# Optimization experiments

Hardware: AMD Instinct MI355X
Metric: run time of the kernel (lower is better)

## Reference

```python
import jax, jax.numpy as jnp
import numpy as np

B, D, S, F, C, H, OUT = 4, 60, 512, 158, 64, 128, 1
LN_EPS = 1e-5


def setup_inputs() -> dict:
    key = jax.random.key(0)
    ks = jax.random.split(key, 12)
    g = lambda k, shape, s=0.05: jax.random.normal(k, shape, dtype=jnp.float32) * s
    return dict(
        x=jax.random.normal(ks[0], (B, D, S, F), dtype=jnp.float32),
        feature_mask=jax.random.randint(ks[1], (B, D, S), 0, 2).astype(bool),
        wq=g(ks[2], (F, C)), bq=jnp.zeros((C,), jnp.float32),
        wk=g(ks[3], (F, C)), bk=jnp.zeros((C,), jnp.float32),
        wv=g(ks[4], (F, C)), bv=jnp.zeros((C,), jnp.float32),
        ln_g=jnp.ones((F + C,), jnp.float32), ln_b=jnp.zeros((F + C,), jnp.float32),
        w_ih=g(ks[5], (3 * H, F + C)), w_hh=g(ks[6], (3 * H, H)),
        b_ih=jnp.zeros((3 * H,), jnp.float32), b_hh=jnp.zeros((3 * H,), jnp.float32),
        w1=g(ks[7], (H, H // 2)), b1=jnp.zeros((H // 2,), jnp.float32),
        w2=g(ks[8], (H // 2, OUT)), b2=jnp.zeros((OUT,), jnp.float32),
    )


def reference(x, feature_mask, wq, bq, wk, bk, wv, bv, ln_g, ln_b,
              w_ih, w_hh, b_ih, b_hh, w1, b1, w2, b2):
    b, d, s, f = x.shape
    c = wq.shape[1]
    h_dim = w_hh.shape[1]

    # --- market context attention, vectorized over (batch, days) ---
    Q = x @ wq + bq            # (B,D,S,C)
    K = x @ wk + bk
    V = x @ wv + bv
    scores = jnp.einsum('bdsc,bdtc->bdst', Q, K) / jnp.sqrt(jnp.float32(c))
    scores = jnp.where(feature_mask[:, :, None, :], scores, -1e9)  # mask keys
    attn = jax.nn.softmax(scores, axis=-1)
    ctx = jnp.einsum('bdst,bdtc->bdsc', attn, V)       # (B,D,S,C)
    ctx = jnp.where(feature_mask[..., None], ctx, 0.0)  # mask queries
    denom = jnp.maximum(feature_mask.sum(axis=2), 1).astype(x.dtype)  # (B,D)
    market = ctx.sum(axis=2) / denom[..., None]         # (B,D,C)

    # --- concat + layernorm ---
    aug = jnp.concatenate(
        [x, jnp.broadcast_to(market[:, :, None, :], (b, d, s, c))], axis=-1)
    mu = aug.mean(-1, keepdims=True)
    var = aug.var(-1, keepdims=True)
    aug = (aug - mu) / jnp.sqrt(var + LN_EPS) * ln_g + ln_b  # (B,D,S,F+C)

    # --- GRU over days, batch = B*S independent sequences ---
    seq = aug.transpose(1, 0, 2, 3).reshape(d, b * s, f + c)  # (D, N, F+C)
    x_proj = seq @ w_ih.T + b_ih                               # (D, N, 3H)

    def step(h, xp):
        hp = h @ w_hh.T + b_hh
        xr, xz, xn = jnp.split(xp, 3, axis=-1)
        hr, hz, hn = jnp.split(hp, 3, axis=-1)
        r = jax.nn.sigmoid(xr + hr)
        z = jax.nn.sigmoid(xz + hz)
        n = jnp.tanh(xn + r * hn)
        return (1.0 - z) * n + z * h, None

    h0 = jnp.zeros((b * s, h_dim), x.dtype)
    h_last, _ = jax.lax.scan(step, h0, x_proj)  # last-step output
    h_last = h_last.reshape(b, s, h_dim)

    # --- output head (dropout inactive in eval) ---
    hid = jax.nn.relu(h_last @ w1 + b1)
    return hid @ w2 + b2  # (B, S, OUT)
```

## Files before the change

kernel.cpp:

```cpp
#include <hip/hip_runtime.h>
#include <hip/hip_bf16.h>
#include <math.h>

#define BB 4
#define DD 60
#define SS 512
#define FF 158
#define CC 64
#define HH 128
#define FC 222
#define G3 384
#define NN 2048
#define BDN 240

typedef _Float16 f16x8 __attribute__((ext_vector_type(8)));
typedef float f32x4 __attribute__((ext_vector_type(4)));

__device__ __forceinline__ float sigmoidf_(float x){ return 1.0f/(1.0f+__expf(-x)); }
__device__ __forceinline__ float tanhf_(float x){
    float e = __expf(-2.0f*fabsf(x));
    float t = (1.0f - e)/(1.0f + e);
    return copysignf(t, x);
}

__global__ void prep_kernel(const float* __restrict__ w_ih,
                            const float* __restrict__ wq, const float* __restrict__ wk,
                            const float* __restrict__ wv,
                            _Float16* __restrict__ wf16, _Float16* __restrict__ wqkv){
    int idx = blockIdx.x*256 + threadIdx.x;
    if (idx < 384*224){
        int n = idx / 224, k = idx % 224;
        wf16[idx] = (k < FC) ? (_Float16)w_ih[n*FC + k] : (_Float16)0.0f;
    } else {
        int i2 = idx - 384*224;
        if (i2 < 192*160){
            int n = i2 / 160, k = i2 % 160;
            float v = 0.0f;
            if (k < FF){
                if (n < 64)       v = wq[k*CC + n];
                else if (n < 128) v = wk[k*CC + (n-64)];
                else              v = wv[k*CC + (n-128)];
            }
            wqkv[i2] = (_Float16)v;
        }
    }
}

__global__ __launch_bounds__(256) void qkv_kernel(const float* __restrict__ x,
                           const _Float16* __restrict__ wqkv,
                           const float* __restrict__ bq, const float* __restrict__ bk,
                           const float* __restrict__ bv,
                           _Float16* __restrict__ Qh, _Float16* __restrict__ Kh,
                           float* __restrict__ V){
    __shared__ _Float16 xa[5][64][40];
    int tid  = threadIdx.x;
    int lane = tid & 63, wv = tid >> 6;
    int col  = lane & 15, quad = lane >> 4;
    int row0 = blockIdx.x * 64;

    f16x8 bfr[3][5];
    #pragma unroll
    for (int nt = 0; nt < 3; ++nt){
        int n = wv*48 + nt*16 + col;
        #pragma unroll
        for (int kq = 0; kq < 5; ++kq)
            bfr[nt][kq] = *(const f16x8*)&wqkv[n*160 + kq*32 + quad*8];
    }

    for (int i = tid; i < 64*160; i += 256){
        int r = i / 160, k = i % 160;
        float v = (k < FF) ? x[(size_t)(row0 + r)*FF + k] : 0.0f;
        xa[k >> 5][r][k & 31] = (_Float16)v;
    }
    __syncthreads();

    float bias[3];
    #pragma unroll
    for (int nt = 0; nt < 3; ++nt){
        int n = wv*48 + nt*16 + col;
        bias[nt] = (n < 64) ? bq[n] : (n < 128 ? bk[n-64] : bv[n-128]);
    }

    #pragma unroll 1
    for (int mt = 0; mt < 4; ++mt){
        f16x8 a[5];
        #pragma unroll
        for (int kq = 0; kq < 5; ++kq)
            a[kq] = *(const f16x8*)&xa[kq][mt*16 + col][quad*8];
        #pragma unroll
        for (int nt = 0; nt < 3; ++nt){
            f32x4 c = {0.0f, 0.0f, 0.0f, 0.0f};
            #pragma unroll
            for (int kq = 0; kq < 5; ++kq)
                c = __builtin_amdgcn_mfma_f32_16x16x32_f16(a[kq], bfr[nt][kq], c, 0, 0, 0);
            int n = wv*48 + nt*16 + col;
            #pragma unroll
            for (int reg = 0; reg < 4; ++reg){
                int row = row0 + mt*16 + quad*4 + reg;
                float val = c[reg] + bias[nt];
                if (n < 64)       Qh[(size_t)row*CC + n]       = (_Float16)val;
                else if (n < 128) Kh[(size_t)row*CC + (n-64)]  = (_Float16)val;
                else              V [(size_t)row*CC + (n-128)] = val;
            }
        }
    }
}

__global__ __launch_bounds__(512) void attn_kernel(const _Float16* __restrict__ Qh,
                                                   const _Float16* __restrict__ Kh,
                                                   const int* __restrict__ mask,
                                                   float* __restrict__ Wg){
    __shared__ _Float16 kf[2][512][32];
    __shared__ float w_sh[512];
    __shared__ float mk_lds[512];

    int tid  = threadIdx.x;
    int bd   = blockIdx.x;
    int lane = tid & 63, wv = tid >> 6;
    int col  = lane & 15, quad = lane >> 4;

    const _Float16* qb = Qh + (size_t)(bd*SS)*CC;
    const _Float16* kb = Kh + (size_t)(bd*SS)*CC;

    {
        int t = tid;
        w_sh[t] = 0.0f;
        mk_lds[t] = (mask[bd*SS + t] != 0) ? 1.0f : 0.0f;
    }
    for (int i = tid; i < 4096; i += 512){
        int t = i >> 3, ch = i & 7;
        *(f16x8*)&kf[ch >> 2][t][(ch & 3)*8] = *(const f16x8*)&kb[t*CC + ch*8];
    }

    f16x8 a0[4], a1[4];
    #pragma unroll
    for (int af = 0; af < 4; ++af){
        int row = wv*64 + af*16 + col;
        a0[af] = *(const f16x8*)&qb[row*CC + quad*8];
        a1[af] = *(const f16x8*)&qb[row*CC + 32 + quad*8];
    }
    __syncthreads();

    float lacc[4][4] = {{0,0,0,0},{0,0,0,0},{0,0,0,0},{0,0,0,0}};
    #pragma unroll 2
    for (int kt = 0; kt < 32; ++kt){
        f16x8 b0 = *(const f16x8*)&kf[0][kt*16 + col][quad*8];
        f16x8 b1 = *(const f16x8*)&kf[1][kt*16 + col][quad*8];
        float mkv = mk_lds[kt*16 + col];
        #pragma unroll
        for (int af = 0; af < 4; ++af){
            f32x4 c = {0.0f, 0.0f, 0.0f, 0.0f};
            c = __builtin_amdgcn_mfma_f32_16x16x32_f16(a0[af], b0, c, 0, 0, 0);
            c = __builtin_amdgcn_mfma_f32_16x16x32_f16(a1[af], b1, c, 0, 0, 0);
            #pragma unroll
            for (int reg = 0; reg < 4; ++reg)
                lacc[af][reg] += __expf(c[reg]*0.125f) * mkv;
        }
    }
    float crv[4][4];
    #pragma unroll
    for (int af = 0; af < 4; ++af){
        #pragma unroll
        for (int reg = 0; reg < 4; ++reg){
            float l = lacc[af][reg];
            l += __shfl_xor(l, 1, 64);
            l += __shfl_xor(l, 2, 64);
            l += __shfl_xor(l, 4, 64);
            l += __shfl_xor(l, 8, 64);
            int row = wv*64 + af*16 + quad*4 + reg;
            crv[af][reg] = mk_lds[row] / l;
        }
    }

    #pragma unroll 2
    for (int kt = 0; kt < 32; ++kt){
        f16x8 b0 = *(const f16x8*)&kf[0][kt*16 + col][quad*8];
        f16x8 b1 = *(const f16x8*)&kf[1][kt*16 + col][quad*8];
        float s = 0.0f;
        #pragma unroll
        for (int af = 0; af < 4; ++af){
            f32x4 c = {0.0f, 0.0f, 0.0f, 0.0f};
            c = __builtin_amdgcn_mfma_f32_16x16x32_f16(a0[af], b0, c, 0, 0, 0);
            c = __builtin_amdgcn_mfma_f32_16x16x32_f16(a1[af], b1, c, 0, 0, 0);
            #pragma unroll
            for (int reg = 0; reg < 4; ++reg)
                s = fmaf(__expf(c[reg]*0.125f), crv[af][reg], s);
        }
        s += __shfl_xor(s, 16, 64);
        s += __shfl_xor(s, 32, 64);
        if (quad == 0)
            atomicAdd(&w_sh[kt*16 + col], s);
    }
    __syncthreads();
    Wg[bd*SS + tid] = w_sh[tid];
}

__global__ void market_kernel(const float* __restrict__ Wg, const float* __restrict__ V,
                              const int* __restrict__ mask, float* __restrict__ market){
    int bd = blockIdx.x;
    int c  = threadIdx.x;
    int cnt = 0;
    #pragma unroll
    for (int j = 0; j < 8; ++j) cnt += (mask[bd*SS + c + j*64] != 0) ? 1 : 0;
    #pragma unroll
    for (int o = 1; o < 64; o <<= 1) cnt += __shfl_xor(cnt, o, 64);
    float acc = 0.0f;
    for (int t = 0; t < SS; ++t){
        float mkt = (mask[bd*SS + t] != 0) ? 1.0f : 0.0f;
        acc = fmaf(Wg[bd*SS + t]*mkt, V[(size_t)(bd*SS + t)*CC + c], acc);
    }
    int dn = cnt < 1 ? 1 : cnt;
    market[bd*CC + c] = acc / (float)dn;
}

__global__ __launch_bounds__(512, 2) void xproj_kernel(const float* __restrict__ x,
                             const float* __restrict__ market,
                             const float* __restrict__ ln_g, const float* __restrict__ ln_b,
                             const _Float16* __restrict__ wf16, const float* __restrict__ b_ih,
                             _Float16* __restrict__ XP){
    __shared__ _Float16 aug[7][64][32];
    int tid  = threadIdx.x;
    int lane = tid & 63, wv = tid >> 6;
    int col  = lane & 15, quad = lane >> 4;
    int row0 = blockIdx.x * 64;

    f16x8 bfr[3][7];
    #pragma unroll
    for (int nt = 0; nt < 3; ++nt){
        int n = wv*48 + nt*16 + col;
        #pragma unroll
        for (int kq = 0; kq < 7; ++kq)
            bfr[nt][kq] = *(const f16x8*)&wf16[n*224 + kq*32 + quad*8];
    }

    {
        int wrow = wv*8 + (lane >> 3);
        int g    = lane & 7;
        int row  = row0 + wrow;
        int d = row / NN, n = row % NN;
        int b = n >> 9, s = n & 511;
        const float* xr = &x[((size_t)((b*DD + d)*SS) + s)*FF];
        const float* mr = &market[(b*DD + d)*CC];
        float v[28];
        float sum = 0.0f, sq = 0.0f;
        #pragma unroll
        for (int j = 0; j < 28; ++j){
            int f = g + 8*j;
            float vv = 0.0f;
            if (f < FF) vv = xr[f];
            else if (f < FC) vv = mr[f - FF];
            v[j] = vv;
            sum += vv; sq += vv*vv;
        }
        sum += __shfl_xor(sum,1,64); sq += __shfl_xor(sq,1,64);
        sum += __shfl_xor(sum,2,64); sq += __shfl_xor(sq,2,64);
        sum += __shfl_xor(sum,4,64); sq += __shfl_xor(sq,4,64);
        float mu   = sum * (1.0f/222.0f);
        float var  = sq * (1.0f/222.0f) - mu*mu;
        float rstd = rsqrtf(var + 1e-5f);
        #pragma unroll
        for (int j = 0; j < 28; ++j){
            int f = g + 8*j;
            float val = (f < FC) ? ((v[j]-mu)*rstd*ln_g[f] + ln_b[f]) : 0.0f;
            aug[f>>5][wrow][f&31] = (_Float16)val;
        }
    }
    __syncthreads();

    float bias[3];
    #pragma unroll
    for (int nt = 0; nt < 3; ++nt) bias[nt] = b_ih[wv*48 + nt*16 + col];
    #pragma unroll 1
    for (int mt = 0; mt < 4; ++mt){
        f16x8 a[7];
        #pragma unroll
        for (int kq = 0; kq < 7; ++kq)
            a[kq] = *(const f16x8*)&aug[kq][mt*16 + col][quad*8];
        #pragma unroll
        for (int nt = 0; nt < 3; ++nt){
            f32x4 c = {0.0f, 0.0f, 0.0f, 0.0f};
            #pragma unroll
            for (int kq = 0; kq < 7; ++kq)
                c = __builtin_amdgcn_mfma_f32_16x16x32_f16(a[kq], bfr[nt][kq], c, 0, 0, 0);
            int nn = wv*48 + nt*16 + col;
            #pragma unroll
            for (int reg = 0; reg < 4; ++reg){
                int m = quad*4 + reg;
                XP[(size_t)(row0 + mt*16 + m)*G3 + nn] = (_Float16)(c[reg] + bias[nt]);
            }
        }
    }
}

__global__ __launch_bounds__(256, 2) void gru_kernel(const _Float16* __restrict__ XP,
                                                     const float* __restrict__ w_hh,
                                                     const float* __restrict__ b_hh,
                                                     const float* __restrict__ w1, const float* __restrict__ b1,
                                                     const float* __restrict__ w2, const float* __restrict__ b2,
                                                     float* __restrict__ out){
    __shared__ _Float16 h_hf[16][136];
    __shared__ float hp_lds[4][392];
    __shared__ float h_f32[4][132];

    int tid  = threadIdx.x;
    int lane = tid & 63, wv = tid >> 6;
    int col  = lane & 15, quad = lane >> 4;
    int row0 = blockIdx.x * 4;

    for (int i = tid; i < 16*136; i += 256) ((_Float16*)h_hf)[i] = (_Float16)0.0f;
    for (int i = tid; i < 4*132; i += 256) ((float*)h_f32)[i] = 0.0f;

    f16x8 bfr[6][4];
    #pragma unroll
    for (int nt = 0; nt < 6; ++nt){
        int n = wv*96 + nt*16 + col;
        #pragma unroll
        for (int kq = 0; kq < 4; ++kq){
            const float* wr = w_hh + n*HH + kq*32 + quad*8;
            f16x8 v;
            #pragma unroll
            for (int j = 0; j < 8; ++j) v[j] = (_Float16)wr[j];
            bfr[nt][kq] = v;
        }
    }

    int cc = tid & 127, sgrp = tid >> 7;
    float bhr = b_hh[cc], bhz = b_hh[128 + cc], bhn = b_hh[256 + cc];

    float xc[2][3], xn_[2][3];
    {
        const _Float16* base = XP + (size_t)(row0)*G3 + cc;
        #pragma unroll
        for (int sp = 0; sp < 2; ++sp){
            int seq = sgrp + 2*sp;
            xc[sp][0] = (float)base[seq*G3];
            xc[sp][1] = (float)base[seq*G3 + 128];
            xc[sp][2] = (float)base[seq*G3 + 256];
        }
    }
    __syncthreads();

    for (int d = 0; d < DD; ++d){
        if (d < DD-1){
            const _Float16* base = XP + ((size_t)(d+1)*NN + row0)*G3 + cc;
            #pragma unroll
            for (int sp = 0; sp < 2; ++sp){
                int seq = sgrp + 2*sp;
                xn_[sp][0] = (float)base[seq*G3];
                xn_[sp][1] = (float)base[seq*G3 + 128];
                xn_[sp][2] = (float)base[seq*G3 + 256];
            }
        }
        f16x8 a[4];
        #pragma unroll
        for (int kq = 0; kq < 4; ++kq)
            a[kq] = *(const f16x8*)&h_hf[col][kq*32 + quad*8];
        f32x4 acc[6];
        #pragma unroll
        for (int nt = 0; nt < 6; ++nt){
            f32x4 c = {0.0f, 0.0f, 0.0f, 0.0f};
            #pragma unroll
            for (int kq = 0; kq < 4; ++kq)
                c = __builtin_amdgcn_mfma_f32_16x16x32_f16(a[kq], bfr[nt][kq], c, 0, 0, 0);
            acc[nt] = c;
        }
        if (quad == 0){
            #pragma unroll
            for (int nt = 0; nt < 6; ++nt){
                int n0 = wv*96 + nt*16 + col;
                #pragma unroll
                for (int reg = 0; reg < 4; ++reg)
                    hp_lds[reg][n0] = acc[nt][reg];
            }
        }
        __syncthreads();
        #pragma unroll
        for (int sp = 0; sp < 2; ++sp){
            int seq = sgrp + 2*sp;
            float hr = hp_lds[seq][cc]       + bhr;
            float hz = hp_lds[seq][cc + 128] + bhz;
            float hn = hp_lds[seq][cc + 256] + bhn;
            float r  = sigmoidf_(xc[sp][0] + hr);
            float z  = sigmoidf_(xc[sp][1] + hz);
            float n  = tanhf_(xc[sp][2] + r*hn);
            float ho = h_f32[seq][cc];
            float hnew = (1.0f - z)*n + z*ho;
            h_f32[seq][cc] = hnew;
            h_hf[seq][cc]  = (_Float16)hnew;
        }
        #pragma unroll
        for (int sp = 0; sp < 2; ++sp){
            xc[sp][0] = xn_[sp][0]; xc[sp][1] = xn_[sp][1]; xc[sp][2] = xn_[sp][2];
        }
        __syncthreads();
    }

    if (tid < 64){
        int c2 = tid;
        #pragma unroll 1
        for (int r = 0; r < 4; ++r){
            float a0 = 0.0f, a1 = 0.0f;
            #pragma unroll 8
            for (int k = 0; k < 64; ++k){
                a0 = fmaf(h_f32[r][k],      w1[k*64 + c2],        a0);
                a1 = fmaf(h_f32[r][64 + k], w1[(64 + k)*64 + c2], a1);
            }
            float hid = fmaxf(a0 + a1 + b1[c2], 0.0f);
            float o = hid * w2[c2];
            #pragma unroll
            for (int off = 1; off < 64; off <<= 1) o += __shfl_xor(o, off, 64);
            if (c2 == 0) out[row0 + r] = o + b2[0];
        }
    }
}

extern "C" void kernel_launch(void* const* d_in, const int* in_sizes, int n_in,
                              void* d_out, int out_size, void* d_ws, size_t ws_size,
                              hipStream_t stream) {
    const float* x    = (const float*)d_in[0];
    const int*   mask = (const int*)d_in[1];
    const float* wq   = (const float*)d_in[2];
    const float* bq   = (const float*)d_in[3];
    const float* wk   = (const float*)d_in[4];
    const float* bk   = (const float*)d_in[5];
    const float* wv   = (const float*)d_in[6];
    const float* bv   = (const float*)d_in[7];
    const float* ln_g = (const float*)d_in[8];
    const float* ln_b = (const float*)d_in[9];
    const float* w_ih = (const float*)d_in[10];
    const float* w_hh = (const float*)d_in[11];
    const float* b_ih = (const float*)d_in[12];
    const float* b_hh = (const float*)d_in[13];
    const float* w1   = (const float*)d_in[14];
    const float* b1   = (const float*)d_in[15];
    const float* w2   = (const float*)d_in[16];
    const float* b2   = (const float*)d_in[17];

    float* ws = (float*)d_ws;
    _Float16* Qh  = (_Float16*)ws;
    _Float16* Kh  = (_Float16*)(ws + 3932160);
    float*    V   = ws + 7864320;
    float*    Wg  = ws + 15728640;
    _Float16* XP  = (_Float16*)ws;
    float* market = ws + 23592960;
    _Float16* wf16= (_Float16*)(ws + 23608320);
    _Float16* wqkv= (_Float16*)(ws + 23651328);

    prep_kernel<<<456, 256, 0, stream>>>(w_ih, wq, wk, wv, wf16, wqkv);
    qkv_kernel<<<1920, 256, 0, stream>>>(x, wqkv, bq, bk, bv, Qh, Kh, V);
    attn_kernel<<<240, 512, 0, stream>>>(Qh, Kh, mask, Wg);
    market_kernel<<<240, 64, 0, stream>>>(Wg, V, mask, market);
    xproj_kernel<<<1920, 512, 0, stream>>>(x, market, ln_g, ln_b, wf16, b_ih, XP);
    gru_kernel<<<512, 256, 0, stream>>>(XP, w_hh, b_hh, w1, b1, w2, b2, (float*)d_out);
}
```

Before: 399.7 us.

## Fuse market reduction into attention and restructure GRU step to one barrier

Folds the separate market-averaging kernel into the tail of the attention kernel, which removes the Wg round-trip through global memory and one launch. The GRU recurrence now gives each wave the r/z/n gate columns for its own 32 hidden units. Per-step hidden state is double-buffered in LDS and kept in registers, cutting one __syncthreads per step. The recurrent weights are pre-converted to fp16 in the prep kernel, so the GRU loads them with vector loads instead of converting from float.

```diff
diff --git a/kernel.cpp b/kernel.cpp
--- a/kernel.cpp
+++ b/kernel.cpp
@@ -25,24 +25,27 @@
 
 __global__ void prep_kernel(const float* __restrict__ w_ih,
                             const float* __restrict__ wq, const float* __restrict__ wk,
-                            const float* __restrict__ wv,
-                            _Float16* __restrict__ wf16, _Float16* __restrict__ wqkv){
+                            const float* __restrict__ wv, const float* __restrict__ w_hh,
+                            _Float16* __restrict__ wf16, _Float16* __restrict__ wqkv,
+                            _Float16* __restrict__ whh16){
     int idx = blockIdx.x*256 + threadIdx.x;
     if (idx < 384*224){
         int n = idx / 224, k = idx % 224;
         wf16[idx] = (k < FC) ? (_Float16)w_ih[n*FC + k] : (_Float16)0.0f;
+    } else if (idx < 384*224 + 192*160){
+        int i2 = idx - 384*224;
+        int n = i2 / 160, k = i2 % 160;
+        float v = 0.0f;
+        if (k < FF){
+            if (n < 64)       v = wq[k*CC + n];
+            else if (n < 128) v = wk[k*CC + (n-64)];
+            else              v = wv[k*CC + (n-128)];
+        }
+        wqkv[i2] = (_Float16)v;
     } else {
-        int i2 = idx - 384*224;
-        if (i2 < 192*160){
-            int n = i2 / 160, k = i2 % 160;
-            float v = 0.0f;
-            if (k < FF){
-                if (n < 64)       v = wq[k*CC + n];
-                else if (n < 128) v = wk[k*CC + (n-64)];
-                else              v = wv[k*CC + (n-128)];
-            }
-            wqkv[i2] = (_Float16)v;
-        }
+        int i3 = idx - (384*224 + 192*160);
+        if (i3 < 384*128)
+            whh16[i3] = (_Float16)w_hh[i3];
     }
 }
 
@@ -109,7 +112,8 @@
 __global__ __launch_bounds__(512) void attn_kernel(const _Float16* __restrict__ Qh,
                                                    const _Float16* __restrict__ Kh,
                                                    const int* __restrict__ mask,
-                                                   float* __restrict__ Wg){
+                                                   const float* __restrict__ V,
+                                                   float* __restrict__ market){
     __shared__ _Float16 kf[2][512][32];
     __shared__ float w_sh[512];
     __shared__ float mk_lds[512];
@@ -192,25 +196,30 @@
             atomicAdd(&w_sh[kt*16 + col], s);
     }
     __syncthreads();
-    Wg[bd*SS + tid] = w_sh[tid];
-}
-
-__global__ void market_kernel(const float* __restrict__ Wg, const float* __restrict__ V,
-                              const int* __restrict__ mask, float* __restrict__ market){
-    int bd = blockIdx.x;
-    int c  = threadIdx.x;
-    int cnt = 0;
-    #pragma unroll
-    for (int j = 0; j < 8; ++j) cnt += (mask[bd*SS + c + j*64] != 0) ? 1 : 0;
-    #pragma unroll
-    for (int o = 1; o < 64; o <<= 1) cnt += __shfl_xor(cnt, o, 64);
-    float acc = 0.0f;
-    for (int t = 0; t < SS; ++t){
-        float mkt = (mask[bd*SS + t] != 0) ? 1.0f : 0.0f;
-        acc = fmaf(Wg[bd*SS + t]*mkt, V[(size_t)(bd*SS + t)*CC + c], acc);
-    }
-    int dn = cnt < 1 ? 1 : cnt;
-    market[bd*CC + c] = acc / (float)dn;
+
+    float* msum = (float*)kf;
+    {
+        int c = tid & 63, grp = tid >> 6;
+        const float* vb = V + (size_t)(bd*SS)*CC;
+        float acc = 0.0f;
+        int t0 = grp*64;
+        #pragma unroll 4
+        for (int t = t0; t < t0 + 64; ++t)
+            acc = fmaf(w_sh[t]*mk_lds[t], vb[(size_t)t*CC + c], acc);
+        msum[grp*64 + c] = acc;
+    }
+    __syncthreads();
+    if (tid < 64){
+        float s = 0.0f;
+        #pragma unroll
+        for (int g = 0; g < 8; ++g) s += msum[g*64 + tid];
+        float cnt = 0.0f;
+        #pragma unroll
+        for (int j = 0; j < 8; ++j) cnt += mk_lds[tid + 64*j];
+        #pragma unroll
+        for (int o = 1; o < 64; o <<= 1) cnt += __shfl_xor(cnt, o, 64);
+        market[bd*CC + tid] = s / fmaxf(cnt, 1.0f);
+    }
 }
 
 __global__ __launch_bounds__(512, 2) void xproj_kernel(const float* __restrict__ x,
@@ -293,13 +302,13 @@
 }
 
 __global__ __launch_bounds__(256, 2) void gru_kernel(const _Float16* __restrict__ XP,
-                                                     const float* __restrict__ w_hh,
+                                                     const _Float16* __restrict__ whh16,
                                                      const float* __restrict__ b_hh,
                                                      const float* __restrict__ w1, const float* __restrict__ b1,
                                                      const float* __restrict__ w2, const float* __restrict__ b2,
                                                      float* __restrict__ out){
-    __shared__ _Float16 h_hf[16][136];
-    __shared__ float hp_lds[4][392];
+    __shared__ _Float16 hfrag[2][4][16][32];
+    __shared__ float hp_sh[4][3][4][32];
     __shared__ float h_f32[4][132];
 
     int tid  = threadIdx.x;
@@ -307,93 +316,94 @@
     int col  = lane & 15, quad = lane >> 4;
     int row0 = blockIdx.x * 4;
 
-    for (int i = tid; i < 16*136; i += 256) ((_Float16*)h_hf)[i] = (_Float16)0.0f;
-    for (int i = tid; i < 4*132; i += 256) ((float*)h_f32)[i] = 0.0f;
-
-    f16x8 bfr[6][4];
-    #pragma unroll
-    for (int nt = 0; nt < 6; ++nt){
-        int n = wv*96 + nt*16 + col;
-        #pragma unroll
-        for (int kq = 0; kq < 4; ++kq){
-            const float* wr = w_hh + n*HH + kq*32 + quad*8;
-            f16x8 v;
-            #pragma unroll
-            for (int j = 0; j < 8; ++j) v[j] = (_Float16)wr[j];
-            bfr[nt][kq] = v;
-        }
-    }
-
-    int cc = tid & 127, sgrp = tid >> 7;
-    float bhr = b_hh[cc], bhz = b_hh[128 + cc], bhn = b_hh[256 + cc];
-
+    for (int i = tid; i < 2*4*16*32; i += 256) ((_Float16*)hfrag)[i] = (_Float16)0.0f;
+
+    f16x8 bfr[3][2][4];
+    #pragma unroll
+    for (int g = 0; g < 3; ++g){
+        #pragma unroll
+        for (int hf = 0; hf < 2; ++hf){
+            int n = g*128 + wv*32 + hf*16 + col;
+            #pragma unroll
+            for (int kq = 0; kq < 4; ++kq)
+                bfr[g][hf][kq] = *(const f16x8*)&whh16[(size_t)n*HH + kq*32 + quad*8];
+        }
+    }
+
+    int u  = lane & 31;
+    int cc = wv*32 + u;
+    int sb = lane >> 5;
+    float bh0 = b_hh[cc], bh1 = b_hh[128 + cc], bh2 = b_hh[256 + cc];
+
+    float hcur[2] = {0.0f, 0.0f};
     float xc[2][3], xn_[2][3];
-    {
-        const _Float16* base = XP + (size_t)(row0)*G3 + cc;
-        #pragma unroll
-        for (int sp = 0; sp < 2; ++sp){
-            int seq = sgrp + 2*sp;
-            xc[sp][0] = (float)base[seq*G3];
-            xc[sp][1] = (float)base[seq*G3 + 128];
-            xc[sp][2] = (float)base[seq*G3 + 256];
-        }
+    #pragma unroll
+    for (int j = 0; j < 2; ++j){
+        int seq = j*2 + sb;
+        const _Float16* base = XP + (size_t)(row0 + seq)*G3 + cc;
+        xc[j][0] = (float)base[0];
+        xc[j][1] = (float)base[128];
+        xc[j][2] = (float)base[256];
     }
     __syncthreads();
 
     for (int d = 0; d < DD; ++d){
         if (d < DD-1){
-            const _Float16* base = XP + ((size_t)(d+1)*NN + row0)*G3 + cc;
-            #pragma unroll
-            for (int sp = 0; sp < 2; ++sp){
-                int seq = sgrp + 2*sp;
-                xn_[sp][0] = (float)base[seq*G3];
-                xn_[sp][1] = (float)base[seq*G3 + 128];
-                xn_[sp][2] = (float)base[seq*G3 + 256];
+            #pragma unroll
+            for (int j = 0; j < 2; ++j){
+                int seq = j*2 + sb;
+                const _Float16* base = XP + ((size_t)(d+1)*NN + row0 + seq)*G3 + cc;
+                xn_[j][0] = (float)base[0];
+                xn_[j][1] = (float)base[128];
+                xn_[j][2] = (float)base[256];
             }
         }
+        int rb = d & 1;
         f16x8 a[4];
         #pragma unroll
         for (int kq = 0; kq < 4; ++kq)
-            a[kq] = *(const f16x8*)&h_hf[col][kq*32 + quad*8];
-        f32x4 acc[6];
-        #pragma unroll
-        for (int nt = 0; nt < 6; ++nt){
-            f32x4 c = {0.0f, 0.0f, 0.0f, 0.0f};
-            #pragma unroll
-            for (int kq = 0; kq < 4; ++kq)
-                c = __builtin_amdgcn_mfma_f32_16x16x32_f16(a[kq], bfr[nt][kq], c, 0, 0, 0);
-            acc[nt] = c;
-        }
-        if (quad == 0){
-            #pragma unroll
-            for (int nt = 0; nt < 6; ++nt){
-                int n0 = wv*96 + nt*16 + col;
+            a[kq] = *(const f16x8*)&hfrag[rb][kq][col][quad*8];
+        #pragma unroll
+        for (int g = 0; g < 3; ++g){
+            #pragma unroll
+            for (int hf = 0; hf < 2; ++hf){
+                f32x4 c = {0.0f, 0.0f, 0.0f, 0.0f};
                 #pragma unroll
-                for (int reg = 0; reg < 4; ++reg)
-                    hp_lds[reg][n0] = acc[nt][reg];
+                for (int kq = 0; kq < 4; ++kq)
+                    c = __builtin_amdgcn_mfma_f32_16x16x32_f16(a[kq], bfr[g][hf][kq], c, 0, 0, 0);
+                if (quad == 0){
+                    #pragma unroll
+                    for (int reg = 0; reg < 4; ++reg)
+                        hp_sh[wv][g][reg][hf*16 + col] = c[reg];
+                }
             }
         }
+        #pragma unroll
+        for (int j = 0; j < 2; ++j){
+            int seq = j*2 + sb;
+            float hr = hp_sh[wv][0][seq][u] + bh0;
+            float hz = hp_sh[wv][1][seq][u] + bh1;
+            float hn = hp_sh[wv][2][seq][u] + bh2;
+            float r  = sigmoidf_(xc[j][0] + hr);
+            float z  = sigmoidf_(xc[j][1] + hz);
+            float n  = tanhf_(xc[j][2] + r*hn);
+            float hnew = (1.0f - z)*n + z*hcur[j];
+            hcur[j] = hnew;
+            hfrag[1 - rb][wv][seq][u] = (_Float16)hnew;
+        }
+        #pragma unroll
+        for (int j = 0; j < 2; ++j){
+            xc[j][0] = xn_[j][0]; xc[j][1] = xn_[j][1]; xc[j][2] = xn_[j][2];
+        }
         __syncthreads();
-        #pragma unroll
-        for (int sp = 0; sp < 2; ++sp){
-            int seq = sgrp + 2*sp;
-            float hr = hp_lds[seq][cc]       + bhr;
-            float hz = hp_lds[seq][cc + 128] + bhz;
-            float hn = hp_lds[seq][cc + 256] + bhn;
-            float r  = sigmoidf_(xc[sp][0] + hr);
-            float z  = sigmoidf_(xc[sp][1] + hz);
-            float n  = tanhf_(xc[sp][2] + r*hn);
-            float ho = h_f32[seq][cc];
-            float hnew = (1.0f - z)*n + z*ho;
-            h_f32[seq][cc] = hnew;
-            h_hf[seq][cc]  = (_Float16)hnew;
-        }
-        #pragma unroll
-        for (int sp = 0; sp < 2; ++sp){
-            xc[sp][0] = xn_[sp][0]; xc[sp][1] = xn_[sp][1]; xc[sp][2] = xn_[sp][2];
-        }
-        __syncthreads();
-    }
+    }
+
+    #pragma unroll
+    for (int j = 0; j < 2; ++j){
+        int seq = j*2 + sb;
+        h_f32[seq][cc] = hcur[j];
+    }
+    __syncthreads();
 
     if (tid < 64){
         int c2 = tid;
@@ -440,16 +450,15 @@
     _Float16* Qh  = (_Float16*)ws;
     _Float16* Kh  = (_Float16*)(ws + 3932160);
     float*    V   = ws + 7864320;
-    float*    Wg  = ws + 15728640;
     _Float16* XP  = (_Float16*)ws;
     float* market = ws + 23592960;
-    _Float16* wf16= (_Float16*)(ws + 23608320);
-    _Float16* wqkv= (_Float16*)(ws + 23651328);
-
-    prep_kernel<<<456, 256, 0, stream>>>(w_ih, wq, wk, wv, wf16, wqkv);
+    _Float16* wf16 = (_Float16*)(ws + 23608320);
+    _Float16* wqkv = (_Float16*)(ws + 23651328);
+    _Float16* whh16= (_Float16*)(ws + 23666688);
+
+    prep_kernel<<<648, 256, 0, stream>>>(w_ih, wq, wk, wv, w_hh, wf16, wqkv, whh16);
     qkv_kernel<<<1920, 256, 0, stream>>>(x, wqkv, bq, bk, bv, Qh, Kh, V);
-    attn_kernel<<<240, 512, 0, stream>>>(Qh, Kh, mask, Wg);
-    market_kernel<<<240, 64, 0, stream>>>(Wg, V, mask, market);
+    attn_kernel<<<240, 512, 0, stream>>>(Qh, Kh, mask, V, market);
     xproj_kernel<<<1920, 512, 0, stream>>>(x, market, ln_g, ln_b, wf16, b_ih, XP);
-    gru_kernel<<<512, 256, 0, stream>>>(XP, w_hh, b_hh, w1, b1, w2, b2, (float*)d_out);
-}
+    gru_kernel<<<512, 256, 0, stream>>>(XP, whh16, b_hh, w1, b1, w2, b2, (float*)d_out);
+}
```

Measured after the change: 367.7 us. -8.0%, faster.
